# Kernel optimization log

Measured on AMD Instinct MI355X. Metric: run time of the kernel, lower is better.

## Reference

```python
import jax, jax.numpy as jnp
import numpy as np

B, T, V, D, K, H = 8, 1024, 256, 4096, 8192, 512
DECAY = 0.95
LN_EPS = 1e-5


def setup_inputs() -> dict:
    key = jax.random.key(0)
    ks = jax.random.split(key, 12)
    cb = jnp.sign(jax.random.normal(ks[0], (V, D), dtype=jnp.float32))
    cb = jnp.where(cb == 0, 1.0, cb)  # bipolar {-1,+1}
    s = 0.02
    return {
        'idx': jax.random.randint(ks[1], (B, T), 0, V, dtype=jnp.int32),
        'char_codebook': cb,
        'mem_keys': s * jax.random.normal(ks[2], (K, D), dtype=jnp.float32),
        'mem_values': s * jax.random.normal(ks[3], (K, H), dtype=jnp.float32),
        'proj_w': s * jax.random.normal(ks[4], (D, H), dtype=jnp.float32),
        'proj_b': jnp.zeros((H,), jnp.float32),
        'res_embed': s * jax.random.normal(ks[5], (V, H), dtype=jnp.float32),
        'pos_embed': s * jax.random.normal(ks[6], (1024, H), dtype=jnp.float32),
        'ln_g': jnp.ones((3 * H,), jnp.float32),
        'ln_b': jnp.zeros((3 * H,), jnp.float32),
        'w1': s * jax.random.normal(ks[7], (3 * H, H), dtype=jnp.float32),
        'b1': jnp.zeros((H,), jnp.float32),
        'w2': s * jax.random.normal(ks[8], (H, H), dtype=jnp.float32),
        'b2': jnp.zeros((H,), jnp.float32),
        'w3': s * jax.random.normal(ks[9], (H, H), dtype=jnp.float32),
        'b3': jnp.zeros((H,), jnp.float32),
        'head_w': s * jax.random.normal(ks[10], (H, V), dtype=jnp.float32),
        'head_b': jnp.zeros((V,), jnp.float32),
    }


def _decay_matrix(t, dtype):
    i = jnp.arange(t)
    diffs = (i[:, None] - i[None, :]).astype(dtype)
    m = jnp.tril(DECAY ** jnp.clip(diffs, 0, None))
    return m / jnp.sum(m, axis=-1, keepdims=True)  # (T,T)


def _layernorm(x, g, b):
    mu = jnp.mean(x, axis=-1, keepdims=True)
    var = jnp.var(x, axis=-1, keepdims=True)
    return (x - mu) * jax.lax.rsqrt(var + LN_EPS) * g + b


def _forward(idx, char_codebook, mem_keys, mem_values, proj_w, proj_b,
             res_embed, pos_embed, ln_g, ln_b, w1, b1, w2, b2, w3, b3,
             head_w, head_b):
    # 1. trigram HDC encoding (bind + roll)
    chars = char_codebook[idx]                       # (B,T,D)
    cm1 = jnp.roll(chars, 1, axis=1).at[:, 0, :].set(0.0)
    cm2 = jnp.roll(chars, 2, axis=1).at[:, :2, :].set(0.0)
    cm1 = jnp.roll(cm1, 1, axis=-1)
    cm2 = jnp.roll(cm2, 2, axis=-1)
    hdc_chars = 0.7 * (chars * cm1 * cm2) + 0.3 * chars
    # 2. causal exponential-decay context: (T,T)@(B,T,D)
    dm = _decay_matrix(hdc_chars.shape[1], hdc_chars.dtype)
    ctx = jnp.einsum('ts,bsd->btd', dm, hdc_chars)   # (B,T,D)
    # 3. associative-memory retrieval over codebook K
    scores = jnp.einsum('btd,kd->btk', ctx, mem_keys) * (D ** -0.5)
    attn = jax.nn.softmax(scores, axis=-1)           # (B,T,K)
    retrieved = jnp.einsum('btk,kh->bth', attn, mem_values)
    # 4. combine + navigator MLP (eval mode: dropout off)
    hdc_float = ctx @ proj_w + proj_b                # (B,T,H)
    residual = res_embed[idx] + pos_embed[:idx.shape[1]]
    x = jnp.concatenate([hdc_float, retrieved, residual], axis=-1)
    x = _layernorm(x, ln_g, ln_b)
    x = jax.nn.gelu(x @ w1 + b1, approximate=False)
    x = jax.nn.gelu(x @ w2 + b2, approximate=False)
    x = jax.nn.gelu(x @ w3 + b3, approximate=False)
    return x @ head_w + head_b                       # (B,T,V) logits


def reference(idx, char_codebook, mem_keys, mem_values, proj_w, proj_b,
              res_embed, pos_embed, ln_g, ln_b, w1, b1, w2, b2, w3, b3,
              head_w, head_b):
    return _forward(idx, char_codebook, mem_keys, mem_values, proj_w, proj_b,
                    res_embed, pos_embed, ln_g, ln_b, w1, b1, w2, b2, w3, b3,
                    head_w, head_b)
```

## Files before the change

### kernel.cpp

```cpp
#include <hip/hip_runtime.h>
#include <hip/hip_bf16.h>

#define BB 8
#define TT 1024
#define VV 256
#define DD 4096
#define KK 8192
#define HH 512
#define MM (BB*TT)

typedef __bf16 v8bf __attribute__((ext_vector_type(8)));
typedef float f32x4 __attribute__((ext_vector_type(4)));

__device__ __forceinline__ void gld16(const void* g, void* l) {
    __builtin_amdgcn_global_load_lds((const __attribute__((address_space(1))) void*)g,
                                     (__attribute__((address_space(3))) void*)l, 16, 0, 0);
}

__device__ __forceinline__ unsigned short bf16bits(float f) {
    __hip_bfloat16 h = __float2bfloat16(f);
    return *reinterpret_cast<unsigned short*>(&h);
}

__global__ __launch_bounds__(256) void cvt_bf16_v4(const float4* __restrict__ in,
                                                   ushort4* __restrict__ out, int n4) {
    int i = blockIdx.x * blockDim.x + threadIdx.x;
    int st = gridDim.x * blockDim.x;
    for (; i < n4; i += st) {
        float4 v = in[i];
        ushort4 o;
        o.x = bf16bits(v.x); o.y = bf16bits(v.y);
        o.z = bf16bits(v.z); o.w = bf16bits(v.w);
        out[i] = o;
    }
}

__global__ __launch_bounds__(256) void transpose_cvt(const float* __restrict__ in,
                                                     __hip_bfloat16* __restrict__ out,
                                                     int R, int C) {
    __shared__ float tile[32][33];
    const int tx = threadIdx.x, ty = threadIdx.y;
    const int c0 = blockIdx.x * 32, r0 = blockIdx.y * 32;
#pragma unroll
    for (int i = ty; i < 32; i += 8)
        tile[i][tx] = in[(size_t)(r0 + i) * C + c0 + tx];
    __syncthreads();
#pragma unroll
    for (int i = ty; i < 32; i += 8)
        out[(size_t)(c0 + i) * R + r0 + tx] = __float2bfloat16(tile[tx][i]);
}

__global__ __launch_bounds__(256)
void hdc_scan(const int* __restrict__ idx, const float* __restrict__ cb,
              __hip_bfloat16* __restrict__ ctx) {
    const int d = blockIdx.x * 256 + threadIdx.x;
    const int chunk = blockIdx.y, b = blockIdx.z;
    const int CL = TT / 8;
    const int t_start = chunk * CL, t_end = t_start + CL;
    int t0 = t_start - 256; if (t0 < 0) t0 = 0;
    const int* ib = idx + b * TT;
    const int dm1 = (d + DD - 1) & (DD - 1);
    const int dm2 = (d + DD - 2) & (DD - 1);
    int i1 = (t0 >= 1) ? ib[t0 - 1] : 0;
    int i2 = (t0 >= 2) ? ib[t0 - 2] : 0;
    float acc = 0.f;
    float dpow = powf(0.95f, (float)(t0 + 1));
    for (int t = t0; t < t_end; ++t) {
        const int it = ib[t];
        const float c0 = cb[(size_t)it * DD + d];
        float h;
        if (t >= 2) {
            const float c1 = cb[(size_t)i1 * DD + dm1];
            const float c2 = cb[(size_t)i2 * DD + dm2];
            h = c0 * (0.7f * c1 * c2 + 0.3f);
        } else {
            h = 0.3f * c0;
        }
        acc = 0.95f * acc + h;
        if (t >= t_start) {
            const float norm = (1.f - dpow) * 20.f;
            ctx[((size_t)b * TT + t) * DD + d] = __float2bfloat16(acc / norm);
        }
        dpow *= 0.95f;
        i2 = i1; i1 = it;
    }
}

__device__ __forceinline__ void stage_tile(const __hip_bfloat16* __restrict__ G, int ld,
                                           int row0, int k0,
                                           __hip_bfloat16* sbuf, int tid) {
    const int w = tid >> 6;
#pragma unroll
    for (int j = 0; j < 2; ++j) {
        const int f = j * 2048 + tid * 8;
        const int r = f >> 5, c = f & 31;
        gld16((const void*)(G + (size_t)(row0 + r) * ld + k0 + c),
              (void*)((char*)sbuf + j * 4096 + w * 1024));
    }
}

template<int OUT_BF16, int DO_GELU>
__global__ __launch_bounds__(256, 2)
void gemm_nt(const __hip_bfloat16* __restrict__ A,
             const __hip_bfloat16* __restrict__ Bm,
             void* __restrict__ Cp,
             const float* __restrict__ bias,
             int M, int N, int Kin, float alpha) {
    __shared__ __hip_bfloat16 sA[2][128 * 32];
    __shared__ __hip_bfloat16 sB[2][128 * 32];
    const int tid = threadIdx.x;
    const int lane = tid & 63, w = tid >> 6;
    const int wm = w >> 1, wn = w & 1;
    const int m0 = blockIdx.y * 128, n0 = blockIdx.x * 128;
    const int nk = Kin >> 5;

    f32x4 acc[4][4];
#pragma unroll
    for (int i = 0; i < 4; ++i)
#pragma unroll
        for (int j = 0; j < 4; ++j) acc[i][j] = f32x4{0.f, 0.f, 0.f, 0.f};

    stage_tile(A, Kin, m0, 0, &sA[0][0], tid);
    stage_tile(Bm, Kin, n0, 0, &sB[0][0], tid);

    const int row = lane & 15, ko8 = (lane >> 4) << 3;
    int p = 0;
    for (int kt = 0; kt < nk; ++kt) {
        __syncthreads();
        if (kt + 1 < nk) {
            stage_tile(A, Kin, m0, (kt + 1) << 5, &sA[p ^ 1][0], tid);
            stage_tile(Bm, Kin, n0, (kt + 1) << 5, &sB[p ^ 1][0], tid);
        }
        v8bf af[4], bfv[4];
#pragma unroll
        for (int f = 0; f < 4; ++f) {
            af[f]  = *reinterpret_cast<const v8bf*>(&sA[p][(wm * 64 + f * 16 + row) * 32 + ko8]);
            bfv[f] = *reinterpret_cast<const v8bf*>(&sB[p][(wn * 64 + f * 16 + row) * 32 + ko8]);
        }
#pragma unroll
        for (int i = 0; i < 4; ++i)
#pragma unroll
            for (int j = 0; j < 4; ++j)
                acc[i][j] = __builtin_amdgcn_mfma_f32_16x16x32_bf16(af[i], bfv[j], acc[i][j], 0, 0, 0);
        p ^= 1;
    }

    const int r4 = (lane >> 4) << 2, col = lane & 15;
#pragma unroll
    for (int i = 0; i < 4; ++i) {
#pragma unroll
        for (int j = 0; j < 4; ++j) {
            const int gn = n0 + wn * 64 + j * 16 + col;
            const float bv = bias ? bias[gn] : 0.f;
#pragma unroll
            for (int q = 0; q < 4; ++q) {
                const int gm = m0 + wm * 64 + i * 16 + r4 + q;
                float v = acc[i][j][q] * alpha + bv;
                if (DO_GELU) v = 0.5f * v * (1.f + erff(v * 0.70710678118f));
                if (OUT_BF16)
                    ((__hip_bfloat16*)Cp)[(size_t)gm * N + gn] = __float2bfloat16(v);
                else
                    ((float*)Cp)[(size_t)gm * N + gn] = v;
            }
        }
    }
}

__global__ __launch_bounds__(256)
void softmax_rows(__hip_bfloat16* __restrict__ S) {
    __shared__ float red[8];
    const int tid = threadIdx.x, lane = tid & 63, w = tid >> 6;
    unsigned short* Sp = reinterpret_cast<unsigned short*>(S);
    const size_t base = (size_t)blockIdx.x * KK;
    float v[32];
    float mx = -1e30f;
#pragma unroll
    for (int i = 0; i < 4; ++i) {
        const int e = (i * 256 + tid) * 8;
        uint4 raw = *reinterpret_cast<const uint4*>(Sp + base + e);
        const unsigned short* u = reinterpret_cast<const unsigned short*>(&raw);
#pragma unroll
        for (int k = 0; k < 8; ++k) {
            const float f = __bfloat162float(*(const __hip_bfloat16*)&u[k]);
            v[i * 8 + k] = f;
            mx = fmaxf(mx, f);
        }
    }
#pragma unroll
    for (int o = 32; o > 0; o >>= 1) mx = fmaxf(mx, __shfl_xor(mx, o, 64));
    if (lane == 0) red[w] = mx;
    __syncthreads();
    mx = fmaxf(fmaxf(red[0], red[1]), fmaxf(red[2], red[3]));
    float sum = 0.f;
#pragma unroll
    for (int k = 0; k < 32; ++k) { v[k] = expf(v[k] - mx); sum += v[k]; }
#pragma unroll
    for (int o = 32; o > 0; o >>= 1) sum += __shfl_xor(sum, o, 64);
    __syncthreads();
    if (lane == 0) red[4 + w] = sum;
    __syncthreads();
    const float inv = 1.f / (red[4] + red[5] + red[6] + red[7]);
#pragma unroll
    for (int i = 0; i < 4; ++i) {
        const int e = (i * 256 + tid) * 8;
        unsigned short ob[8];
#pragma unroll
        for (int k = 0; k < 8; ++k) ob[k] = bf16bits(v[i * 8 + k] * inv);
        *reinterpret_cast<uint4*>(Sp + base + e) = *reinterpret_cast<const uint4*>(ob);
    }
}

__global__ __launch_bounds__(256)
void ln_concat(const float* __restrict__ hdcf, const float* __restrict__ retr,
               const int* __restrict__ idx, const float* __restrict__ res_embed,
               const float* __restrict__ pos_embed, const float* __restrict__ g,
               const float* __restrict__ bta, __hip_bfloat16* __restrict__ xln) {
    __shared__ float red[8];
    const int row = blockIdx.x, tid = threadIdx.x;
    const int lane = tid & 63, w = tid >> 6;
    const int t = row & (TT - 1);
    const int i0 = idx[row];
    float vals[6];
    float s = 0.f, sq = 0.f;
#pragma unroll
    for (int i = 0; i < 6; ++i) {
        const int e = i * 256 + tid;
        float v;
        if (i < 2)      v = hdcf[(size_t)row * HH + e];
        else if (i < 4) v = retr[(size_t)row * HH + (e - HH)];
        else            v = res_embed[(size_t)i0 * HH + (e - 2 * HH)]
                          + pos_embed[(size_t)t * HH + (e - 2 * HH)];
        vals[i] = v; s += v; sq += v * v;
    }
#pragma unroll
    for (int o = 32; o > 0; o >>= 1) { s += __shfl_xor(s, o, 64); sq += __shfl_xor(sq, o, 64); }
    if (lane == 0) { red[w] = s; red[4 + w] = sq; }
    __syncthreads();
    s  = red[0] + red[1] + red[2] + red[3];
    sq = red[4] + red[5] + red[6] + red[7];
    const float mu  = s * (1.f / 1536.f);
    const float var = sq * (1.f / 1536.f) - mu * mu;
    const float is  = rsqrtf(var + 1e-5f);
#pragma unroll
    for (int i = 0; i < 6; ++i) {
        const int e = i * 256 + tid;
        xln[(size_t)row * 1536 + e] = __float2bfloat16((vals[i] - mu) * is * g[e] + bta[e]);
    }
}

extern "C" void kernel_launch(void* const* d_in, const int* in_sizes, int n_in,
                              void* d_out, int out_size, void* d_ws, size_t ws_size,
                              hipStream_t stream) {
    const int*   idx       = (const int*)d_in[0];
    const float* cb        = (const float*)d_in[1];
    const float* mem_keys  = (const float*)d_in[2];
    const float* mem_vals  = (const float*)d_in[3];
    const float* proj_w    = (const float*)d_in[4];
    const float* proj_b    = (const float*)d_in[5];
    const float* res_embed = (const float*)d_in[6];
    const float* pos_embed = (const float*)d_in[7];
    const float* ln_g      = (const float*)d_in[8];
    const float* ln_b      = (const float*)d_in[9];
    const float* w1        = (const float*)d_in[10];
    const float* b1        = (const float*)d_in[11];
    const float* w2        = (const float*)d_in[12];
    const float* b2        = (const float*)d_in[13];
    const float* w3        = (const float*)d_in[14];
    const float* b3        = (const float*)d_in[15];
    const float* head_w    = (const float*)d_in[16];
    const float* head_b    = (const float*)d_in[17];

    size_t off = 0;
    auto alloc = [&](size_t bytes) {
        void* p = (char*)d_ws + off;
        off += (bytes + 255) & ~(size_t)255;
        return p;
    };
    __hip_bfloat16* ctx   = (__hip_bfloat16*)alloc((size_t)MM * DD * 2);
    __hip_bfloat16* keysb = (__hip_bfloat16*)alloc((size_t)KK * DD * 2);
    __hip_bfloat16* S     = (__hip_bfloat16*)alloc((size_t)MM * KK * 2);
    __hip_bfloat16* valT  = (__hip_bfloat16*)alloc((size_t)HH * KK * 2);
    __hip_bfloat16* projT = (__hip_bfloat16*)alloc((size_t)HH * DD * 2);
    __hip_bfloat16* w1T   = (__hip_bfloat16*)alloc((size_t)HH * 1536 * 2);
    __hip_bfloat16* w2T   = (__hip_bfloat16*)alloc((size_t)HH * HH * 2);
    __hip_bfloat16* w3T   = (__hip_bfloat16*)alloc((size_t)HH * HH * 2);
    __hip_bfloat16* hwT   = (__hip_bfloat16*)alloc((size_t)VV * HH * 2);
    float* hdcf           = (float*)alloc((size_t)MM * HH * 4);
    float* retr           = (float*)alloc((size_t)MM * HH * 4);
    __hip_bfloat16* xln   = (__hip_bfloat16*)alloc((size_t)MM * 1536 * 2);
    __hip_bfloat16* h1    = (__hip_bfloat16*)alloc((size_t)MM * HH * 2);
    __hip_bfloat16* h2    = (__hip_bfloat16*)alloc((size_t)MM * HH * 2);
    __hip_bfloat16* h3    = h1;

    cvt_bf16_v4<<<2048, 256, 0, stream>>>((const float4*)mem_keys, (ushort4*)keysb,
                                          KK * DD / 4);
    dim3 tb(32, 8);
    transpose_cvt<<<dim3(HH / 32, KK / 32), tb, 0, stream>>>(mem_vals, valT, KK, HH);
    transpose_cvt<<<dim3(HH / 32, DD / 32), tb, 0, stream>>>(proj_w, projT, DD, HH);
    transpose_cvt<<<dim3(HH / 32, 1536 / 32), tb, 0, stream>>>(w1, w1T, 1536, HH);
    transpose_cvt<<<dim3(HH / 32, HH / 32), tb, 0, stream>>>(w2, w2T, HH, HH);
    transpose_cvt<<<dim3(HH / 32, HH / 32), tb, 0, stream>>>(w3, w3T, HH, HH);
    transpose_cvt<<<dim3(VV / 32, HH / 32), tb, 0, stream>>>(head_w, hwT, HH, VV);
    hdc_scan<<<dim3(DD / 256, 8, BB), 256, 0, stream>>>(idx, cb, ctx);
    gemm_nt<1, 0><<<dim3(KK / 128, MM / 128), 256, 0, stream>>>(
        ctx, keysb, S, nullptr, MM, KK, DD, 0.015625f);
    softmax_rows<<<MM, 256, 0, stream>>>(S);
    gemm_nt<0, 0><<<dim3(HH / 128, MM / 128), 256, 0, stream>>>(
        S, valT, retr, nullptr, MM, HH, KK, 1.f);
    gemm_nt<0, 0><<<dim3(HH / 128, MM / 128), 256, 0, stream>>>(
        ctx, projT, hdcf, proj_b, MM, HH, DD, 1.f);
    ln_concat<<<MM, 256, 0, stream>>>(hdcf, retr, idx, res_embed, pos_embed,
                                      ln_g, ln_b, xln);
    gemm_nt<1, 1><<<dim3(HH / 128, MM / 128), 256, 0, stream>>>(
        xln, w1T, h1, b1, MM, HH, 1536, 1.f);
    gemm_nt<1, 1><<<dim3(HH / 128, MM / 128), 256, 0, stream>>>(
        h1, w2T, h2, b2, MM, HH, HH, 1.f);
    gemm_nt<1, 1><<<dim3(HH / 128, MM / 128), 256, 0, stream>>>(
        h2, w3T, h3, b3, MM, HH, HH, 1.f);
    gemm_nt<0, 0><<<dim3(VV / 128, MM / 128), 256, 0, stream>>>(
        h3, hwT, (float*)d_out, head_b, MM, VV, HH, 1.f);
}
```

Baseline: 1.505 ms.

## Add 256x256 eight-wave ping-pong GEMM for the score matmul

Adds a new bf16 MFMA GEMM kernel with 256x256 output tiles, 512 threads and double-buffered LDS fed by direct global-to-LDS loads. The K loop is split into four phases whose loads are interleaved with MFMA blocks, using barriers and s_setprio, plus an XCD-aware remapping of block ids. Only the dominant ctx x mem_keys score GEMM (8192x8192x4096) switches to it, aiming at more reuse per LDS byte and better overlap of memory with compute. The larger tile uses 128 KB of LDS and many accumulator registers, which may limit occupancy despite the launch bound of 2.

Result: slower. 1.536 ms (+2.1%).

```diff
diff --git a/kernel.cpp b/kernel.cpp
--- a/kernel.cpp
+++ b/kernel.cpp
@@ -86,6 +86,123 @@
     }
 }
 
+#define PH_MID() do {                                        \
+    asm volatile("s_barrier" ::: "memory");                  \
+    asm volatile("s_waitcnt lgkmcnt(0)" ::: "memory");       \
+    __builtin_amdgcn_sched_barrier(0);                       \
+    __builtin_amdgcn_s_setprio(1); } while (0)
+#define PH_END() do {                                        \
+    __builtin_amdgcn_s_setprio(0);                           \
+    __builtin_amdgcn_sched_barrier(0);                       \
+    asm volatile("s_barrier" ::: "memory"); } while (0)
+
+#define MFMA16(qm, qn)                                                          \
+    _Pragma("unroll")                                                           \
+    for (int m = 0; m < 4; ++m)                                                 \
+        _Pragma("unroll")                                                       \
+        for (int n = 0; n < 2; ++n) {                                           \
+            acc[(qm)*4+m][(qn)*2+n] = __builtin_amdgcn_mfma_f32_16x16x32_bf16(  \
+                a[m][0], b[qn][n][0], acc[(qm)*4+m][(qn)*2+n], 0, 0, 0);        \
+            acc[(qm)*4+m][(qn)*2+n] = __builtin_amdgcn_mfma_f32_16x16x32_bf16(  \
+                a[m][1], b[qn][n][1], acc[(qm)*4+m][(qn)*2+n], 0, 0, 0);        \
+        }
+
+#define STAGE_A(t, h) do { const int _t = (t);                                          \
+    gld16(A  + rtA + (size_t)((h) * 128) * Kin + _t * 64,                               \
+          &sA[_t & 1][((h) * 16 + w) << 9]);                                            \
+    gld16(A  + rtA + (size_t)((h) * 128 + 64) * Kin + _t * 64,                          \
+          &sA[_t & 1][((h) * 16 + 8 + w) << 9]); } while (0)
+#define STAGE_B(t, h) do { const int _t = (t);                                          \
+    gld16(Bm + rtB + (size_t)((h) * 128) * Kin + _t * 64,                               \
+          &sB[_t & 1][((h) * 16 + w) << 9]);                                            \
+    gld16(Bm + rtB + (size_t)((h) * 128 + 64) * Kin + _t * 64,                          \
+          &sB[_t & 1][((h) * 16 + 8 + w) << 9]); } while (0)
+
+#define FRA(m, kg) (*reinterpret_cast<const v8bf*>(lA + aBase + (m) * 1024 + (kg) * 512))
+#define FRB(j, kg) (*reinterpret_cast<const v8bf*>(lB + bBase + (j) * 1024 + (kg) * 512))
+
+template<int OUT_BF16>
+__global__ __launch_bounds__(512, 2)
+void gemm_nt_8p(const __hip_bfloat16* __restrict__ A,
+                const __hip_bfloat16* __restrict__ Bm,
+                void* __restrict__ Cp, const float* __restrict__ bias,
+                int M, int N, int Kin, float alpha) {
+    __shared__ __hip_bfloat16 sA[2][256 * 64];
+    __shared__ __hip_bfloat16 sB[2][256 * 64];
+    const int tid = threadIdx.x, lane = tid & 63, w = tid >> 6;
+    const int wm = w >> 2, wn = w & 3;
+    int bid = blockIdx.x;
+    const int cpx = gridDim.x >> 3;
+    bid = (bid & 7) * cpx + (bid >> 3);
+    const int nbx = N >> 8;
+    const int m0 = (bid / nbx) << 8, n0 = (bid % nbx) << 8;
+    const int NT = Kin >> 6;
+    const int rowOff = (w >> 1) * 16 + (lane & 15);
+    const int colOff = (w & 1) * 32 + ((lane >> 4) << 3);
+    const size_t rtA = (size_t)(m0 + rowOff) * Kin + colOff;
+    const size_t rtB = (size_t)(n0 + rowOff) * Kin + colOff;
+    const int aBase = wm * 8192 + lane * 8;
+    const int bBase = wn * 4096 + lane * 8;
+
+    f32x4 acc[8][4];
+#pragma unroll
+    for (int i = 0; i < 8; ++i)
+#pragma unroll
+        for (int j = 0; j < 4; ++j) acc[i][j] = f32x4{0.f, 0.f, 0.f, 0.f};
+    v8bf a[4][2], b[2][2][2];
+
+    STAGE_B(0, 0); STAGE_A(0, 0); STAGE_B(0, 1); STAGE_A(0, 1);
+    STAGE_B(1, 0); STAGE_A(1, 0);
+    asm volatile("s_waitcnt vmcnt(4)" ::: "memory");
+    asm volatile("s_barrier" ::: "memory");
+
+    const __hip_bfloat16* lA;
+    const __hip_bfloat16* lB;
+    for (int t = 0; t < NT; ++t) {
+        lA = sA[t & 1]; lB = sB[t & 1];
+#pragma unroll
+        for (int m = 0; m < 4; ++m) { a[m][0] = FRA(m, 0); a[m][1] = FRA(m, 1); }
+#pragma unroll
+        for (int n = 0; n < 2; ++n) { b[0][n][0] = FRB(n, 0); b[0][n][1] = FRB(n, 1); }
+        if (t + 1 < NT) STAGE_B(t + 1, 1);
+        PH_MID(); MFMA16(0, 0); PH_END();
+#pragma unroll
+        for (int n = 0; n < 2; ++n) { b[1][n][0] = FRB(2 + n, 0); b[1][n][1] = FRB(2 + n, 1); }
+        if (t + 1 < NT) STAGE_A(t + 1, 1);
+        PH_MID(); MFMA16(0, 1); PH_END();
+#pragma unroll
+        for (int m = 0; m < 4; ++m) { a[m][0] = FRA(4 + m, 0); a[m][1] = FRA(4 + m, 1); }
+        if (t + 2 < NT) STAGE_B(t + 2, 0);
+        PH_MID(); MFMA16(1, 1); PH_END();
+        if (t + 2 < NT) {
+            STAGE_A(t + 2, 0);
+            asm volatile("s_waitcnt vmcnt(4)" ::: "memory");
+        } else {
+            asm volatile("s_waitcnt vmcnt(0)" ::: "memory");
+        }
+        PH_MID(); MFMA16(1, 0); PH_END();
+    }
+
+    const int r4 = (lane >> 4) << 2, colL = lane & 15;
+#pragma unroll
+    for (int i = 0; i < 8; ++i) {
+#pragma unroll
+        for (int j = 0; j < 4; ++j) {
+            const int gn = n0 + wn * 64 + j * 16 + colL;
+            const float bv = bias ? bias[gn] : 0.f;
+#pragma unroll
+            for (int q = 0; q < 4; ++q) {
+                const int gm = m0 + wm * 128 + i * 16 + r4 + q;
+                float v = acc[i][j][q] * alpha + bv;
+                if (OUT_BF16)
+                    ((__hip_bfloat16*)Cp)[(size_t)gm * N + gn] = __float2bfloat16(v);
+                else
+                    ((float*)Cp)[(size_t)gm * N + gn] = v;
+            }
+        }
+    }
+}
+
 __device__ __forceinline__ void stage_tile(const __hip_bfloat16* __restrict__ G, int ld,
                                            int row0, int k0,
                                            __hip_bfloat16* sbuf, int tid) {
@@ -302,7 +419,7 @@
     transpose_cvt<<<dim3(HH / 32, HH / 32), tb, 0, stream>>>(w3, w3T, HH, HH);
     transpose_cvt<<<dim3(VV / 32, HH / 32), tb, 0, stream>>>(head_w, hwT, HH, VV);
     hdc_scan<<<dim3(DD / 256, 8, BB), 256, 0, stream>>>(idx, cb, ctx);
-    gemm_nt<1, 0><<<dim3(KK / 128, MM / 128), 256, 0, stream>>>(
+    gemm_nt_8p<1><<<dim3((MM / 256) * (KK / 256)), 512, 0, stream>>>(
         ctx, keysb, S, nullptr, MM, KK, DD, 0.015625f);
     softmax_rows<<<MM, 256, 0, stream>>>(S);
     gemm_nt<0, 0><<<dim3(HH / 128, MM / 128), 256, 0, stream>>>(
```

## Quantize context and memory keys to int8 and use i8 MFMA for scores

Applied to the files above, without the earlier changes.

Replaces the bf16 score GEMM (ctx x mem_keys) with an int8 GEMM built on the 16x16x64 i8 MFMA. hdc_scan now also writes an int8 copy of the context, and the keys are quantized with fixed scales. The new kernel uses a grouped block-id remap for L2 locality. This halves operand bytes and doubles nominal MFMA throughput for the dominant GEMM, at the cost of lower score precision from the fixed-scale quantization plus an extra int8 context write.

After: 1.379 ms. -8.4%, faster.

```diff
diff --git a/kernel.cpp b/kernel.cpp
--- a/kernel.cpp
+++ b/kernel.cpp
@@ -11,6 +11,7 @@
 
 typedef __bf16 v8bf __attribute__((ext_vector_type(8)));
 typedef float f32x4 __attribute__((ext_vector_type(4)));
+typedef int   v4i  __attribute__((ext_vector_type(4)));
 
 __device__ __forceinline__ void gld16(const void* g, void* l) {
     __builtin_amdgcn_global_load_lds((const __attribute__((address_space(1))) void*)g,
@@ -22,16 +23,26 @@
     return *reinterpret_cast<unsigned short*>(&h);
 }
 
-__global__ __launch_bounds__(256) void cvt_bf16_v4(const float4* __restrict__ in,
-                                                   ushort4* __restrict__ out, int n4) {
+__device__ __forceinline__ char q8(float v, float s) {
+    int t = __float2int_rn(v * s);
+    t = t > 127 ? 127 : (t < -127 ? -127 : t);
+    return (char)t;
+}
+
+__global__ __launch_bounds__(256) void quant_i8(const float* __restrict__ in,
+                                                char* __restrict__ out, int n16, float s) {
     int i = blockIdx.x * blockDim.x + threadIdx.x;
-    int st = gridDim.x * blockDim.x;
-    for (; i < n4; i += st) {
-        float4 v = in[i];
-        ushort4 o;
-        o.x = bf16bits(v.x); o.y = bf16bits(v.y);
-        o.z = bf16bits(v.z); o.w = bf16bits(v.w);
-        out[i] = o;
+    const int st = gridDim.x * blockDim.x;
+    for (; i < n16; i += st) {
+        const float4* p = reinterpret_cast<const float4*>(in) + i * 4;
+        union { char c[16]; int4 v; } u;
+#pragma unroll
+        for (int j = 0; j < 4; ++j) {
+            float4 v = p[j];
+            u.c[j * 4 + 0] = q8(v.x, s); u.c[j * 4 + 1] = q8(v.y, s);
+            u.c[j * 4 + 2] = q8(v.z, s); u.c[j * 4 + 3] = q8(v.w, s);
+        }
+        *reinterpret_cast<int4*>(out + (size_t)i * 16) = u.v;
     }
 }
 
@@ -52,7 +63,7 @@
 
 __global__ __launch_bounds__(256)
 void hdc_scan(const int* __restrict__ idx, const float* __restrict__ cb,
-              __hip_bfloat16* __restrict__ ctx) {
+              __hip_bfloat16* __restrict__ ctx, char* __restrict__ ctxq) {
     const int d = blockIdx.x * 256 + threadIdx.x;
     const int chunk = blockIdx.y, b = blockIdx.z;
     const int CL = TT / 8;
@@ -79,10 +90,85 @@
         acc = 0.95f * acc + h;
         if (t >= t_start) {
             const float norm = (1.f - dpow) * 20.f;
-            ctx[((size_t)b * TT + t) * DD + d] = __float2bfloat16(acc / norm);
+            const float xv = acc / norm;
+            const size_t o = ((size_t)b * TT + t) * DD + d;
+            ctx[o]  = __float2bfloat16(xv);
+            ctxq[o] = q8(xv, 127.f);
         }
         dpow *= 0.95f;
         i2 = i1; i1 = it;
+    }
+}
+
+__device__ __forceinline__ void stage_i8(const char* __restrict__ G, int ld,
+                                         int row0, int k0, char* sbuf,
+                                         int w, int qrow, int qk) {
+#pragma unroll
+    for (int j = 0; j < 2; ++j) {
+        const int s = j * 4 + w;
+        gld16(G + (size_t)(row0 + s * 16 + qrow) * ld + k0 + qk,
+              sbuf + s * 1024);
+    }
+}
+
+__global__ __launch_bounds__(256, 2)
+void gemm_i8_scores(const char* __restrict__ A, const char* __restrict__ Bq,
+                    __hip_bfloat16* __restrict__ S,
+                    int M, int N, int Kin, float scl) {
+    __shared__ char sA[2][8192];
+    __shared__ char sB[2][8192];
+    const int tid = threadIdx.x, lane = tid & 63, w = tid >> 6;
+    const int wm = w >> 1, wn = w & 1;
+    int bid = blockIdx.x;
+    const int cpx = gridDim.x >> 3;
+    bid = (bid & 7) * cpx + (bid >> 3);
+    const int nbx = N >> 7;
+    const int m0 = (bid / nbx) << 7, n0 = (bid % nbx) << 7;
+    const int nk = Kin >> 6;
+    const int qrow = lane & 15, qk = (lane >> 4) << 4;
+
+    v4i acc[4][4];
+#pragma unroll
+    for (int i = 0; i < 4; ++i)
+#pragma unroll
+        for (int j = 0; j < 4; ++j) acc[i][j] = v4i{0, 0, 0, 0};
+
+    stage_i8(A,  Kin, m0, 0, &sA[0][0], w, qrow, qk);
+    stage_i8(Bq, Kin, n0, 0, &sB[0][0], w, qrow, qk);
+
+    int p = 0;
+    for (int kt = 0; kt < nk; ++kt) {
+        __syncthreads();
+        if (kt + 1 < nk) {
+            stage_i8(A,  Kin, m0, (kt + 1) << 6, &sA[p ^ 1][0], w, qrow, qk);
+            stage_i8(Bq, Kin, n0, (kt + 1) << 6, &sB[p ^ 1][0], w, qrow, qk);
+        }
+        v4i a[4], b[4];
+#pragma unroll
+        for (int f = 0; f < 4; ++f) {
+            a[f] = *reinterpret_cast<const v4i*>(&sA[p][(wm * 4 + f) * 1024 + lane * 16]);
+            b[f] = *reinterpret_cast<const v4i*>(&sB[p][(wn * 4 + f) * 1024 + lane * 16]);
+        }
+#pragma unroll
+        for (int i = 0; i < 4; ++i)
+#pragma unroll
+            for (int j = 0; j < 4; ++j)
+                acc[i][j] = __builtin_amdgcn_mfma_i32_16x16x64_i8(a[i], b[j], acc[i][j], 0, 0, 0);
+        p ^= 1;
+    }
+
+    const int r4 = (lane >> 4) << 2, col = lane & 15;
+#pragma unroll
+    for (int i = 0; i < 4; ++i) {
+#pragma unroll
+        for (int j = 0; j < 4; ++j) {
+            const int gn = n0 + wn * 64 + j * 16 + col;
+#pragma unroll
+            for (int q = 0; q < 4; ++q) {
+                const int gm = m0 + wm * 64 + i * 16 + r4 + q;
+                S[(size_t)gm * N + gn] = __float2bfloat16((float)acc[i][j][q] * scl);
+            }
+        }
     }
 }
 
@@ -277,7 +363,8 @@
         return p;
     };
     __hip_bfloat16* ctx   = (__hip_bfloat16*)alloc((size_t)MM * DD * 2);
-    __hip_bfloat16* keysb = (__hip_bfloat16*)alloc((size_t)KK * DD * 2);
+    char* ctxq            = (char*)alloc((size_t)MM * DD);
+    char* keysq           = (char*)alloc((size_t)KK * DD);
     __hip_bfloat16* S     = (__hip_bfloat16*)alloc((size_t)MM * KK * 2);
     __hip_bfloat16* valT  = (__hip_bfloat16*)alloc((size_t)HH * KK * 2);
     __hip_bfloat16* projT = (__hip_bfloat16*)alloc((size_t)HH * DD * 2);
@@ -292,8 +379,7 @@
     __hip_bfloat16* h2    = (__hip_bfloat16*)alloc((size_t)MM * HH * 2);
     __hip_bfloat16* h3    = h1;
 
-    cvt_bf16_v4<<<2048, 256, 0, stream>>>((const float4*)mem_keys, (ushort4*)keysb,
-                                          KK * DD / 4);
+    quant_i8<<<2048, 256, 0, stream>>>(mem_keys, keysq, KK * DD / 16, 1024.f);
     dim3 tb(32, 8);
     transpose_cvt<<<dim3(HH / 32, KK / 32), tb, 0, stream>>>(mem_vals, valT, KK, HH);
     transpose_cvt<<<dim3(HH / 32, DD / 32), tb, 0, stream>>>(proj_w, projT, DD, HH);
@@ -301,9 +387,9 @@
     transpose_cvt<<<dim3(HH / 32, HH / 32), tb, 0, stream>>>(w2, w2T, HH, HH);
     transpose_cvt<<<dim3(HH / 32, HH / 32), tb, 0, stream>>>(w3, w3T, HH, HH);
     transpose_cvt<<<dim3(VV / 32, HH / 32), tb, 0, stream>>>(head_w, hwT, HH, VV);
-    hdc_scan<<<dim3(DD / 256, 8, BB), 256, 0, stream>>>(idx, cb, ctx);
-    gemm_nt<1, 0><<<dim3(KK / 128, MM / 128), 256, 0, stream>>>(
-        ctx, keysb, S, nullptr, MM, KK, DD, 0.015625f);
+    hdc_scan<<<dim3(DD / 256, 8, BB), 256, 0, stream>>>(idx, cb, ctx, ctxq);
+    gemm_i8_scores<<<dim3((MM / 128) * (KK / 128)), 256, 0, stream>>>(
+        ctxq, keysq, S, MM, KK, DD, 1.f / (127.f * 1024.f * 64.f));
     softmax_rows<<<MM, 256, 0, stream>>>(S);
     gemm_nt<0, 0><<<dim3(HH / 128, MM / 128), 256, 0, stream>>>(
         S, valT, retr, nullptr, MM, HH, KK, 1.f);
```
